# Kernel tuning notes

Hardware: AMD Instinct MI355X
Metric: run time of the kernel (lower is better)

Reference implementation:

```python
import jax, jax.numpy as jnp
import numpy as np

H, W, BS, CIN = 224, 608, 1, 128
CLS = (16, 12, 10)
PAD = (0, 2, 3)
C12 = CLS[0] * CLS[1]            # 192
C123 = C12 * CLS[2]              # 1920
SUPER = 384
CFACT = C123 // SUPER            # 5
PAD_PROJ = 0.1


def _p(key, shape):
    return jax.random.normal(key, shape, dtype=jnp.float32) * 0.05


def setup_inputs() -> dict:
    key = jax.random.key(0)
    ks = iter(jax.random.split(key, 32))
    d = {"x_in": jax.random.normal(next(ks), (BS, CIN, H, W), dtype=jnp.float32)}
    # stage-1: grouped 1x1 convs (groups=height -> one [out,in] matmul per image line)
    for i, (ci, co) in enumerate([(32, 32), (32, 32), (32, CLS[0] + 2 * PAD[0])]):
        d[f"w1_{i}"] = _p(next(ks), (H, co, ci))
        d[f"b1_{i}"] = _p(next(ks), (H, co))
    # stage-2: CondMul tables indexed by line*16 + stage-1 class
    for i, (ci, co) in enumerate([(32, 32), (32, 32), (32, CLS[1] + 2 * PAD[1])]):
        d[f"w2_{i}"] = _p(next(ks), (H * CLS[0], ci, co))
        d[f"b2_{i}"] = _p(next(ks), (H * CLS[0], co))
    # stage-3: CondMul tables indexed by line*192 + stage-12 class
    for i, (ci, co) in enumerate([(32, 32), (32, 32), (32, CLS[2] + 2 * PAD[2])]):
        d[f"w3_{i}"] = _p(next(ks), (H * C12, ci, co))
        d[f"b3_{i}"] = _p(next(ks), (H * C12, co))
    d["wr0"] = _p(next(ks), (H * SUPER, 32, 32))
    d["br0"] = _p(next(ks), (H * SUPER, 32))
    d["wr1"] = _p(next(ks), (H * C123, 32, 1))
    d["br1"] = _p(next(ks), (H * C123, 1))
    return d


def _condmul(x, inds, w, b):
    # CondMul: y[n] = x[n] @ w[inds[n]] + b[inds[n]]
    return jnp.einsum('ni,nio->no', x, w[inds]) + b[inds]


def _forward(x_in, w1, b1, w2, b2, w3, b3, wr0, br0, wr1, br1):
    bs, _, h, w_ = x_in.shape
    lrelu = jax.nn.leaky_relu  # negative_slope=0.01, same as torch default
    offsets = jnp.arange(h, dtype=jnp.int32).reshape(1, 1, h, 1)
    # ---- stage 1: per-line 1x1 grouped conv stack -> argmax class
    x = x_in[:, 0:32].transpose(0, 2, 1, 3)                    # [b,h,32,w]
    for i in range(3):
        x = jnp.einsum('bhiw,hoi->bhow', x, w1[i]) + b1[i][None, :, :, None]
        if i < 2:
            x = lrelu(x)
    x = x.transpose(0, 2, 1, 3)                                 # [b,16,h,w]
    inds1 = jnp.argmax(x, axis=1)[:, None].astype(jnp.int32)    # [b,1,h,w]
    inds1_l = (inds1 + CLS[0] * offsets).reshape(-1)
    # ---- stage 2: CondMul chain conditioned on (line, class1)
    x = x_in[:, 32:64].transpose(0, 2, 3, 1).reshape(-1, 32)    # [N,32]
    for i in range(3):
        x = _condmul(x, inds1_l, w2[i], b2[i])
        if i < 2:
            x = lrelu(x)
    inds2 = jnp.argmax(x, axis=1).astype(jnp.int32).reshape(bs, 1, h, w_)
    inds12 = inds1 * CLS[1] + (inds2 - PAD[1])
    inds12_l = (jnp.clip(inds12, 0, C12 - 1) + C12 * offsets).reshape(-1)
    # ---- stage 3: CondMul chain conditioned on (line, class12)
    x = x_in[:, 64:96].transpose(0, 2, 3, 1).reshape(-1, 32)
    for i in range(3):
        if i < 2:
            x = lrelu(_condmul(x, inds12_l, w3[i], b3[i]))
        else:
            x = _condmul(x, inds12_l, w3[i], b3[i])
    inds3 = jnp.argmax(x, axis=1).astype(jnp.int32).reshape(bs, 1, h, w_)
    inds123 = jnp.clip(inds12 * CLS[2] + (inds3 - PAD[2]), 0, C123 - 1)
    inds = inds123.reshape(-1)
    lines = jnp.broadcast_to(offsets, (bs, 1, h, w_)).reshape(-1)
    inds_l = inds + C123 * lines                                 # per-leaf index
    inds_super_l = inds // CFACT + SUPER * lines                 # superclass index (reg_line_div=1)
    x = x_in[:, 96:128].transpose(0, 2, 3, 1).reshape(-1, 32)
    x = lrelu(_condmul(x, inds_super_l, wr0, br0))
    r = _condmul(x, inds_l, wr1, br1)[:, 0]                      # [N]
    out = (inds.astype(jnp.float32) + r).reshape(bs, 1, h, w_) / float(C123)
    out = (out - PAD_PROJ) / (1.0 - 2.0 * PAD_PROJ)              # undo projector padding
    return out


def reference(x_in, w1_0, b1_0, w1_1, b1_1, w1_2, b1_2,
              w2_0, b2_0, w2_1, b2_1, w2_2, b2_2,
              w3_0, b3_0, w3_1, b3_1, w3_2, b3_2,
              wr0, br0, wr1, br1):
    return _forward(x_in,
                    (w1_0, w1_1, w1_2), (b1_0, b1_1, b1_2),
                    (w2_0, w2_1, w2_2), (b2_0, b2_1, b2_2),
                    (w3_0, w3_1, w3_2), (b3_0, b3_1, b3_2),
                    wr0, br0, wr1, br1)
```

## Files before the change

### kernel.cpp

```cpp
#include <hip/hip_runtime.h>
#include <cstddef>

#define HH 224
#define WW 608
#define HWSZ (HH * WW)

__device__ __forceinline__ float lrelu(float v) { return v > 0.0f ? v : 0.01f * v; }

template <int CO>
__device__ __forceinline__ void cm4(const float* __restrict__ wmat,
                                    const float* __restrict__ bvec,
                                    int s, const float (&act)[8], float (&acc)[CO / 4]) {
    constexpr int CH = CO / 4;
#pragma unroll
    for (int j = 0; j < CH; j++) acc[j] = 0.0f;
#pragma unroll
    for (int sp = 0; sp < 4; sp++) {
#pragma unroll
        for (int ii = 0; ii < 8; ii++) {
            float xi = __shfl(act[ii], sp, 4);
            const float* wr = wmat + (sp * 8 + ii) * CO + s * CH;
            if constexpr (CH == 8) {
                float4 a = *reinterpret_cast<const float4*>(wr);
                float4 b = *reinterpret_cast<const float4*>(wr + 4);
                acc[0] = fmaf(xi, a.x, acc[0]); acc[1] = fmaf(xi, a.y, acc[1]);
                acc[2] = fmaf(xi, a.z, acc[2]); acc[3] = fmaf(xi, a.w, acc[3]);
                acc[4] = fmaf(xi, b.x, acc[4]); acc[5] = fmaf(xi, b.y, acc[5]);
                acc[6] = fmaf(xi, b.z, acc[6]); acc[7] = fmaf(xi, b.w, acc[7]);
            } else {
                float4 a = *reinterpret_cast<const float4*>(wr);
                acc[0] = fmaf(xi, a.x, acc[0]); acc[1] = fmaf(xi, a.y, acc[1]);
                acc[2] = fmaf(xi, a.z, acc[2]); acc[3] = fmaf(xi, a.w, acc[3]);
            }
        }
    }
#pragma unroll
    for (int j = 0; j < CH; j++) acc[j] += bvec[s * CH + j];
}

__device__ __forceinline__ void wb_lrelu8(float (&act)[8], const float (&acc)[8]) {
#pragma unroll
    for (int j = 0; j < 8; j++) act[j] = lrelu(acc[j]);
}

__device__ __forceinline__ int argmax4(const float (&v)[4], int s) {
    float bv = v[0];
    int bi = 4 * s;
#pragma unroll
    for (int j = 1; j < 4; j++) {
        if (v[j] > bv) { bv = v[j]; bi = 4 * s + j; }
    }
#pragma unroll
    for (int m = 1; m <= 2; m <<= 1) {
        float ov = __shfl_xor(bv, m, 4);
        int oi = __shfl_xor(bi, m, 4);
        if (ov > bv || (ov == bv && oi < bi)) { bv = ov; bi = oi; }
    }
    return bi;
}

extern "C" __global__ __launch_bounds__(256, 4)
void k_stage1(const float* __restrict__ x_in,
              const float* __restrict__ w1_0, const float* __restrict__ b1_0,
              const float* __restrict__ w1_1, const float* __restrict__ b1_1,
              const float* __restrict__ w1_2, const float* __restrict__ b1_2,
              int* __restrict__ c1out) {
    const int h = blockIdx.y;
    const int tid = threadIdx.x;
    const int p = tid >> 2;
    const int s = tid & 3;
    const int w = blockIdx.x * 64 + p;
    const bool valid = (w < WW);
    const int wc = valid ? w : (WW - 1);
    const int base = h * WW + wc;

    __shared__ __align__(16) float sW0[1024];
    __shared__ __align__(16) float sW1[1024];
    __shared__ __align__(16) float sW2[512];
    for (int tt = tid; tt < 1024; tt += 256) {
        int i = tt >> 5, o = tt & 31;
        sW0[tt] = w1_0[h * 1024 + o * 32 + i];
        sW1[tt] = w1_1[h * 1024 + o * 32 + i];
    }
    for (int tt = tid; tt < 512; tt += 256) {
        int i = tt >> 4, o = tt & 15;
        sW2[tt] = w1_2[h * 512 + o * 32 + i];
    }
    __syncthreads();

    float act[8], acc8[8], acc4[4];
#pragma unroll
    for (int ii = 0; ii < 8; ii++) act[ii] = x_in[(8 * s + ii) * HWSZ + base];
    cm4<32>(sW0, b1_0 + h * 32, s, act, acc8);
    wb_lrelu8(act, acc8);
    cm4<32>(sW1, b1_1 + h * 32, s, act, acc8);
    wb_lrelu8(act, acc8);
    cm4<16>(sW2, b1_2 + h * 16, s, act, acc4);
    const int i1 = argmax4(acc4, s);

    if (s == 0 && valid) c1out[base] = i1;
}

template <int NBINS>
__global__ __launch_bounds__(256)
void k_sort(const int* __restrict__ cls_in, int* __restrict__ perm, int clipmax) {
    const int h = blockIdx.x;
    const int tid = threadIdx.x;
    __shared__ int cls[WW];
    __shared__ int off[NBINS];
    __shared__ int hist[NBINS];
    for (int t = tid; t < NBINS; t += 256) hist[t] = 0;
    __syncthreads();
    for (int t = tid; t < WW; t += 256) {
        int v = cls_in[h * WW + t];
        v = min(max(v, 0), clipmax);
        cls[t] = v;
        atomicAdd(&hist[v], 1);
    }
    __syncthreads();
    if (tid == 0) {
        int run = 0;
        for (int i = 0; i < NBINS; i++) { off[i] = run; run += hist[i]; }
    }
    __syncthreads();
    for (int t = tid; t < WW; t += 256) {
        int pos = atomicAdd(&off[cls[t]], 1);
        perm[h * WW + pos] = t;
    }
}

extern "C" __global__ __launch_bounds__(256, 4)
void k_stage2(const float* __restrict__ x_in,
              const float* __restrict__ w2_0, const float* __restrict__ b2_0,
              const float* __restrict__ w2_1, const float* __restrict__ b2_1,
              const float* __restrict__ w2_2, const float* __restrict__ b2_2,
              const int* __restrict__ c1arr, const int* __restrict__ perm1,
              int* __restrict__ inds12out) {
    const int h = blockIdx.y;
    const int tid = threadIdx.x;
    const int s = tid & 3;
    int pos = blockIdx.x * 64 + (tid >> 2);
    pos = min(pos, WW - 1);
    const int p = perm1[h * WW + pos];
    const int base = h * WW + p;
    const int i1 = c1arr[base];

    float act[8], acc8[8], acc4[4];
#pragma unroll
    for (int ii = 0; ii < 8; ii++) act[ii] = x_in[(32 + 8 * s + ii) * HWSZ + base];
    const size_t idx2 = (size_t)h * 16 + (size_t)i1;
    cm4<32>(w2_0 + idx2 * 1024, b2_0 + idx2 * 32, s, act, acc8);
    wb_lrelu8(act, acc8);
    cm4<32>(w2_1 + idx2 * 1024, b2_1 + idx2 * 32, s, act, acc8);
    wb_lrelu8(act, acc8);
    cm4<16>(w2_2 + idx2 * 512, b2_2 + idx2 * 16, s, act, acc4);
    const int i2 = argmax4(acc4, s);

    if (s == 0) inds12out[base] = i1 * 12 + (i2 - 2);
}

extern "C" __global__ __launch_bounds__(256, 4)
void k_stage3(const float* __restrict__ x_in,
              const float* __restrict__ w3_0, const float* __restrict__ b3_0,
              const float* __restrict__ w3_1, const float* __restrict__ b3_1,
              const float* __restrict__ w3_2, const float* __restrict__ b3_2,
              const float* __restrict__ wr0, const float* __restrict__ br0,
              const float* __restrict__ wr1, const float* __restrict__ br1,
              const int* __restrict__ inds12arr, const int* __restrict__ perm2,
              float* __restrict__ out) {
    const int h = blockIdx.y;
    const int tid = threadIdx.x;
    const int s = tid & 3;
    int pos = blockIdx.x * 64 + (tid >> 2);
    pos = min(pos, WW - 1);
    const int p = perm2[h * WW + pos];
    const int base = h * WW + p;
    const int inds12 = inds12arr[base];
    const int c12 = min(max(inds12, 0), 191);
    const size_t idx3 = (size_t)h * 192 + (size_t)c12;

    float act[8], acc8[8], acc4[4];
#pragma unroll
    for (int ii = 0; ii < 8; ii++) act[ii] = x_in[(64 + 8 * s + ii) * HWSZ + base];
    cm4<32>(w3_0 + idx3 * 1024, b3_0 + idx3 * 32, s, act, acc8);
    wb_lrelu8(act, acc8);
    cm4<32>(w3_1 + idx3 * 1024, b3_1 + idx3 * 32, s, act, acc8);
    wb_lrelu8(act, acc8);
    cm4<16>(w3_2 + idx3 * 512, b3_2 + idx3 * 16, s, act, acc4);
    const int i3 = argmax4(acc4, s);

    const int inds123 = min(max(inds12 * 10 + (i3 - 3), 0), 1919);

#pragma unroll
    for (int ii = 0; ii < 8; ii++) act[ii] = x_in[(96 + 8 * s + ii) * HWSZ + base];
    const size_t idxs = (size_t)h * 384 + (size_t)(inds123 / 5);
    cm4<32>(wr0 + idxs * 1024, br0 + idxs * 32, s, act, acc8);
    wb_lrelu8(act, acc8);

    const size_t idxr = (size_t)h * 1920 + (size_t)inds123;
    const float* __restrict__ wr1r = wr1 + idxr * 32 + 8 * s;
    float4 wa = *reinterpret_cast<const float4*>(wr1r);
    float4 wb = *reinterpret_cast<const float4*>(wr1r + 4);
    float rpart = 0.0f;
    rpart = fmaf(act[0], wa.x, rpart); rpart = fmaf(act[1], wa.y, rpart);
    rpart = fmaf(act[2], wa.z, rpart); rpart = fmaf(act[3], wa.w, rpart);
    rpart = fmaf(act[4], wb.x, rpart); rpart = fmaf(act[5], wb.y, rpart);
    rpart = fmaf(act[6], wb.z, rpart); rpart = fmaf(act[7], wb.w, rpart);
    rpart += __shfl_xor(rpart, 1, 4);
    rpart += __shfl_xor(rpart, 2, 4);
    const float r = rpart + br1[idxr];

    if (s == 0) {
        float v = ((float)inds123 + r) * (1.0f / 1920.0f);
        out[base] = (v - 0.1f) * 1.25f;
    }
}

extern "C" __global__ __launch_bounds__(256, 4)
void regressor_fused(const float* __restrict__ x_in,
                     const float* __restrict__ w1_0, const float* __restrict__ b1_0,
                     const float* __restrict__ w1_1, const float* __restrict__ b1_1,
                     const float* __restrict__ w1_2, const float* __restrict__ b1_2,
                     const float* __restrict__ w2_0, const float* __restrict__ b2_0,
                     const float* __restrict__ w2_1, const float* __restrict__ b2_1,
                     const float* __restrict__ w2_2, const float* __restrict__ b2_2,
                     const float* __restrict__ w3_0, const float* __restrict__ b3_0,
                     const float* __restrict__ w3_1, const float* __restrict__ b3_1,
                     const float* __restrict__ w3_2, const float* __restrict__ b3_2,
                     const float* __restrict__ wr0, const float* __restrict__ br0,
                     const float* __restrict__ wr1, const float* __restrict__ br1,
                     float* __restrict__ out) {
    const int h = blockIdx.y;
    const int tid = threadIdx.x;
    const int p = tid >> 2;
    const int s = tid & 3;
    const int w = blockIdx.x * 64 + p;
    const bool valid = (w < WW);
    const int wc = valid ? w : (WW - 1);
    const int base = h * WW + wc;

    __shared__ __align__(16) float sW0[1024];
    __shared__ __align__(16) float sW1[1024];
    __shared__ __align__(16) float sW2[512];
    for (int tt = tid; tt < 1024; tt += 256) {
        int i = tt >> 5, o = tt & 31;
        sW0[tt] = w1_0[h * 1024 + o * 32 + i];
        sW1[tt] = w1_1[h * 1024 + o * 32 + i];
    }
    for (int tt = tid; tt < 512; tt += 256) {
        int i = tt >> 4, o = tt & 15;
        sW2[tt] = w1_2[h * 512 + o * 32 + i];
    }
    __syncthreads();

    float act[8], acc8[8], acc4[4];
#pragma unroll
    for (int ii = 0; ii < 8; ii++) act[ii] = x_in[(8 * s + ii) * HWSZ + base];
    cm4<32>(sW0, b1_0 + h * 32, s, act, acc8);
    wb_lrelu8(act, acc8);
    cm4<32>(sW1, b1_1 + h * 32, s, act, acc8);
    wb_lrelu8(act, acc8);
    cm4<16>(sW2, b1_2 + h * 16, s, act, acc4);
    const int i1 = argmax4(acc4, s);

#pragma unroll
    for (int ii = 0; ii < 8; ii++) act[ii] = x_in[(32 + 8 * s + ii) * HWSZ + base];
    const size_t idx2 = (size_t)h * 16 + (size_t)i1;
    cm4<32>(w2_0 + idx2 * 1024, b2_0 + idx2 * 32, s, act, acc8);
    wb_lrelu8(act, acc8);
    cm4<32>(w2_1 + idx2 * 1024, b2_1 + idx2 * 32, s, act, acc8);
    wb_lrelu8(act, acc8);
    cm4<16>(w2_2 + idx2 * 512, b2_2 + idx2 * 16, s, act, acc4);
    const int i2 = argmax4(acc4, s);

    const int inds12 = i1 * 12 + (i2 - 2);
    const int c12 = min(max(inds12, 0), 191);
    const size_t idx3 = (size_t)h * 192 + (size_t)c12;

#pragma unroll
    for (int ii = 0; ii < 8; ii++) act[ii] = x_in[(64 + 8 * s + ii) * HWSZ + base];
    cm4<32>(w3_0 + idx3 * 1024, b3_0 + idx3 * 32, s, act, acc8);
    wb_lrelu8(act, acc8);
    cm4<32>(w3_1 + idx3 * 1024, b3_1 + idx3 * 32, s, act, acc8);
    wb_lrelu8(act, acc8);
    cm4<16>(w3_2 + idx3 * 512, b3_2 + idx3 * 16, s, act, acc4);
    const int i3 = argmax4(acc4, s);

    const int inds123 = min(max(inds12 * 10 + (i3 - 3), 0), 1919);

#pragma unroll
    for (int ii = 0; ii < 8; ii++) act[ii] = x_in[(96 + 8 * s + ii) * HWSZ + base];
    const size_t idxs = (size_t)h * 384 + (size_t)(inds123 / 5);
    cm4<32>(wr0 + idxs * 1024, br0 + idxs * 32, s, act, acc8);
    wb_lrelu8(act, acc8);

    const size_t idxr = (size_t)h * 1920 + (size_t)inds123;
    const float* __restrict__ wr1r = wr1 + idxr * 32 + 8 * s;
    float4 wa = *reinterpret_cast<const float4*>(wr1r);
    float4 wb = *reinterpret_cast<const float4*>(wr1r + 4);
    float rpart = 0.0f;
    rpart = fmaf(act[0], wa.x, rpart); rpart = fmaf(act[1], wa.y, rpart);
    rpart = fmaf(act[2], wa.z, rpart); rpart = fmaf(act[3], wa.w, rpart);
    rpart = fmaf(act[4], wb.x, rpart); rpart = fmaf(act[5], wb.y, rpart);
    rpart = fmaf(act[6], wb.z, rpart); rpart = fmaf(act[7], wb.w, rpart);
    rpart += __shfl_xor(rpart, 1, 4);
    rpart += __shfl_xor(rpart, 2, 4);
    const float r = rpart + br1[idxr];

    if (s == 0 && valid) {
        float v = ((float)inds123 + r) * (1.0f / 1920.0f);
        out[h * WW + w] = (v - 0.1f) * 1.25f;
    }
}

extern "C" void kernel_launch(void* const* d_in, const int* in_sizes, int n_in,
                              void* d_out, int out_size, void* d_ws, size_t ws_size,
                              hipStream_t stream) {
    const float* p[23];
    for (int i = 0; i < 23; i++) p[i] = (const float*)d_in[i];
    float* out = (float*)d_out;

    const size_t N = (size_t)HWSZ;
    const size_t need = 4 * N * sizeof(int);

    if (ws_size < need) {
        regressor_fused<<<dim3(10, HH), 256, 0, stream>>>(
            p[0], p[1], p[2], p[3], p[4], p[5], p[6],
            p[7], p[8], p[9], p[10], p[11], p[12],
            p[13], p[14], p[15], p[16], p[17], p[18],
            p[19], p[20], p[21], p[22], out);
        return;
    }

    int* c1 = (int*)d_ws;
    int* perm1 = c1 + N;
    int* inds12 = perm1 + N;
    int* perm2 = inds12 + N;

    dim3 gridMain(10, HH);
    k_stage1<<<gridMain, 256, 0, stream>>>(p[0], p[1], p[2], p[3], p[4], p[5], p[6], c1);
    k_sort<16><<<dim3(HH), 256, 0, stream>>>(c1, perm1, 15);
    k_stage2<<<gridMain, 256, 0, stream>>>(p[0], p[7], p[8], p[9], p[10], p[11], p[12],
                                           c1, perm1, inds12);
    k_sort<192><<<dim3(HH), 256, 0, stream>>>(inds12, perm2, 191);
    k_stage3<<<gridMain, 256, 0, stream>>>(p[0], p[13], p[14], p[15], p[16], p[17], p[18],
                                           p[19], p[20], p[21], p[22],
                                           inds12, perm2, out);
}
```

Before: 157.5 us.

## Physically permute input channels during class sort so stages read contiguously

The sort kernels now gather the needed input channels into a sorted-order workspace buffer, along with the sorted class indices. Stages 2 and 3 can then read activations and class ids with coalesced loads instead of strided gathers through the permutation. Results are scattered back once at the output write. In exchange, a large workspace and extra copy traffic are needed, and the sort kernels run with 1024-thread blocks.

Result: slower. 173.0 us (+9.8%).

```diff
diff --git a/kernel.cpp b/kernel.cpp
--- a/kernel.cpp
+++ b/kernel.cpp
@@ -101,21 +101,27 @@
     if (s == 0 && valid) c1out[base] = i1;
 }
 
-template <int NBINS>
-__global__ __launch_bounds__(256)
-void k_sort(const int* __restrict__ cls_in, int* __restrict__ perm, int clipmax) {
+template <int NBINS, int CH0, int NCH>
+__global__ __launch_bounds__(1024)
+void k_sort_copy(const float* __restrict__ x_in,
+                 const int* __restrict__ cls_in, int clipmax,
+                 int* __restrict__ perm, int* __restrict__ raw_sorted,
+                 float* __restrict__ xs) {
     const int h = blockIdx.x;
     const int tid = threadIdx.x;
-    __shared__ int cls[WW];
+    __shared__ int raw[WW];
+    __shared__ int cclip[WW];
+    __shared__ int perml[WW];
+    __shared__ int hist[NBINS];
     __shared__ int off[NBINS];
-    __shared__ int hist[NBINS];
-    for (int t = tid; t < NBINS; t += 256) hist[t] = 0;
-    __syncthreads();
-    for (int t = tid; t < WW; t += 256) {
+    for (int t = tid; t < NBINS; t += 1024) hist[t] = 0;
+    __syncthreads();
+    for (int t = tid; t < WW; t += 1024) {
         int v = cls_in[h * WW + t];
-        v = min(max(v, 0), clipmax);
-        cls[t] = v;
-        atomicAdd(&hist[v], 1);
+        raw[t] = v;
+        int c = min(max(v, 0), clipmax);
+        cclip[t] = c;
+        atomicAdd(&hist[c], 1);
     }
     __syncthreads();
     if (tid == 0) {
@@ -123,31 +129,41 @@
         for (int i = 0; i < NBINS; i++) { off[i] = run; run += hist[i]; }
     }
     __syncthreads();
-    for (int t = tid; t < WW; t += 256) {
-        int pos = atomicAdd(&off[cls[t]], 1);
-        perm[h * WW + pos] = t;
+    for (int t = tid; t < WW; t += 1024) {
+        int pos = atomicAdd(&off[cclip[t]], 1);
+        perml[pos] = t;
+    }
+    __syncthreads();
+    for (int t = tid; t < WW; t += 1024) {
+        perm[h * WW + t] = perml[t];
+        raw_sorted[h * WW + t] = raw[perml[t]];
+    }
+    for (int idx = tid; idx < NCH * WW; idx += 1024) {
+        int ch = idx / WW;
+        int pos = idx - ch * WW;
+        xs[(size_t)ch * HWSZ + h * WW + pos] =
+            x_in[(size_t)(CH0 + ch) * HWSZ + h * WW + perml[pos]];
     }
 }
 
 extern "C" __global__ __launch_bounds__(256, 4)
-void k_stage2(const float* __restrict__ x_in,
+void k_stage2(const float* __restrict__ xs2,
               const float* __restrict__ w2_0, const float* __restrict__ b2_0,
               const float* __restrict__ w2_1, const float* __restrict__ b2_1,
               const float* __restrict__ w2_2, const float* __restrict__ b2_2,
-              const int* __restrict__ c1arr, const int* __restrict__ perm1,
+              const int* __restrict__ c1s, const int* __restrict__ perm1,
               int* __restrict__ inds12out) {
     const int h = blockIdx.y;
     const int tid = threadIdx.x;
     const int s = tid & 3;
     int pos = blockIdx.x * 64 + (tid >> 2);
     pos = min(pos, WW - 1);
-    const int p = perm1[h * WW + pos];
-    const int base = h * WW + p;
-    const int i1 = c1arr[base];
+    const int spos = h * WW + pos;
+    const int i1 = c1s[spos];
 
     float act[8], acc8[8], acc4[4];
 #pragma unroll
-    for (int ii = 0; ii < 8; ii++) act[ii] = x_in[(32 + 8 * s + ii) * HWSZ + base];
+    for (int ii = 0; ii < 8; ii++) act[ii] = xs2[(size_t)(8 * s + ii) * HWSZ + spos];
     const size_t idx2 = (size_t)h * 16 + (size_t)i1;
     cm4<32>(w2_0 + idx2 * 1024, b2_0 + idx2 * 32, s, act, acc8);
     wb_lrelu8(act, acc8);
@@ -156,32 +172,31 @@
     cm4<16>(w2_2 + idx2 * 512, b2_2 + idx2 * 16, s, act, acc4);
     const int i2 = argmax4(acc4, s);
 
-    if (s == 0) inds12out[base] = i1 * 12 + (i2 - 2);
+    if (s == 0) inds12out[h * WW + perm1[spos]] = i1 * 12 + (i2 - 2);
 }
 
 extern "C" __global__ __launch_bounds__(256, 4)
-void k_stage3(const float* __restrict__ x_in,
+void k_stage3(const float* __restrict__ xs3,
               const float* __restrict__ w3_0, const float* __restrict__ b3_0,
               const float* __restrict__ w3_1, const float* __restrict__ b3_1,
               const float* __restrict__ w3_2, const float* __restrict__ b3_2,
               const float* __restrict__ wr0, const float* __restrict__ br0,
               const float* __restrict__ wr1, const float* __restrict__ br1,
-              const int* __restrict__ inds12arr, const int* __restrict__ perm2,
+              const int* __restrict__ r12s, const int* __restrict__ perm2,
               float* __restrict__ out) {
     const int h = blockIdx.y;
     const int tid = threadIdx.x;
     const int s = tid & 3;
     int pos = blockIdx.x * 64 + (tid >> 2);
     pos = min(pos, WW - 1);
-    const int p = perm2[h * WW + pos];
-    const int base = h * WW + p;
-    const int inds12 = inds12arr[base];
+    const int spos = h * WW + pos;
+    const int inds12 = r12s[spos];
     const int c12 = min(max(inds12, 0), 191);
     const size_t idx3 = (size_t)h * 192 + (size_t)c12;
 
     float act[8], acc8[8], acc4[4];
 #pragma unroll
-    for (int ii = 0; ii < 8; ii++) act[ii] = x_in[(64 + 8 * s + ii) * HWSZ + base];
+    for (int ii = 0; ii < 8; ii++) act[ii] = xs3[(size_t)(8 * s + ii) * HWSZ + spos];
     cm4<32>(w3_0 + idx3 * 1024, b3_0 + idx3 * 32, s, act, acc8);
     wb_lrelu8(act, acc8);
     cm4<32>(w3_1 + idx3 * 1024, b3_1 + idx3 * 32, s, act, acc8);
@@ -192,7 +207,7 @@
     const int inds123 = min(max(inds12 * 10 + (i3 - 3), 0), 1919);
 
 #pragma unroll
-    for (int ii = 0; ii < 8; ii++) act[ii] = x_in[(96 + 8 * s + ii) * HWSZ + base];
+    for (int ii = 0; ii < 8; ii++) act[ii] = xs3[(size_t)(32 + 8 * s + ii) * HWSZ + spos];
     const size_t idxs = (size_t)h * 384 + (size_t)(inds123 / 5);
     cm4<32>(wr0 + idxs * 1024, br0 + idxs * 32, s, act, acc8);
     wb_lrelu8(act, acc8);
@@ -212,7 +227,7 @@
 
     if (s == 0) {
         float v = ((float)inds123 + r) * (1.0f / 1920.0f);
-        out[base] = (v - 0.1f) * 1.25f;
+        out[h * WW + perm2[spos]] = (v - 0.1f) * 1.25f;
     }
 }
 
@@ -321,7 +336,7 @@
     float* out = (float*)d_out;
 
     const size_t N = (size_t)HWSZ;
-    const size_t need = 4 * N * sizeof(int);
+    const size_t need = (6 + 32 + 64) * N * sizeof(float);
 
     if (ws_size < need) {
         regressor_fused<<<dim3(10, HH), 256, 0, stream>>>(
@@ -334,16 +349,20 @@
 
     int* c1 = (int*)d_ws;
     int* perm1 = c1 + N;
-    int* inds12 = perm1 + N;
+    int* c1s = perm1 + N;
+    int* inds12 = c1s + N;
     int* perm2 = inds12 + N;
+    int* r12s = perm2 + N;
+    float* xs2 = (float*)(r12s + N);
+    float* xs3 = xs2 + 32 * N;
 
     dim3 gridMain(10, HH);
     k_stage1<<<gridMain, 256, 0, stream>>>(p[0], p[1], p[2], p[3], p[4], p[5], p[6], c1);
-    k_sort<16><<<dim3(HH), 256, 0, stream>>>(c1, perm1, 15);
-    k_stage2<<<gridMain, 256, 0, stream>>>(p[0], p[7], p[8], p[9], p[10], p[11], p[12],
-                                           c1, perm1, inds12);
-    k_sort<192><<<dim3(HH), 256, 0, stream>>>(inds12, perm2, 191);
-    k_stage3<<<gridMain, 256, 0, stream>>>(p[0], p[13], p[14], p[15], p[16], p[17], p[18],
+    k_sort_copy<16, 32, 32><<<dim3(HH), 1024, 0, stream>>>(p[0], c1, 15, perm1, c1s, xs2);
+    k_stage2<<<gridMain, 256, 0, stream>>>(xs2, p[7], p[8], p[9], p[10], p[11], p[12],
+                                           c1s, perm1, inds12);
+    k_sort_copy<192, 64, 64><<<dim3(HH), 1024, 0, stream>>>(p[0], inds12, 191, perm2, r12s, xs3);
+    k_stage3<<<gridMain, 256, 0, stream>>>(xs3, p[13], p[14], p[15], p[16], p[17], p[18],
                                            p[19], p[20], p[21], p[22],
-                                           inds12, perm2, out);
-}
+                                           r12s, perm2, out);
+}
```
